# Kernel optimization log

Hardware: AMD Instinct MI355X
Metric: run time of the kernel (lower is better)

The kernel has to match this reference:

```python
import jax, jax.numpy as jnp
import numpy as np

P = 7            # POOL_SIZE
NUM_CLASSES = 20
STRIDE = 16      # FEATURE_STRIDE
SCALE = 1.0 / STRIDE
C_IN = 512
C_MID = 2 * C_IN
C_CLS = P * P * (NUM_CLASSES + 1)        # 1029
C_BOX = P * P * (NUM_CLASSES + 1) * 4    # 4116
H, W = 38, 50
K = 300
IMG_H, IMG_W = 600.0, 800.0


def conv1x1(w, b, x):
    # w: [Cout, Cin], b: [Cout], x: [Cin, H, W] -> ReLU(conv) (CNNBlock = Conv2d 1x1 + ReLU)
    return jax.nn.relu(jnp.einsum('oi,ihw->ohw', w, x) + b[:, None, None])


def ps_roi_pool(maps, rois_xyxy):
    # maps: [Ctot, H, W] with Ctot = Cout*P*P, channel index = (c*P + ph)*P + pw
    # rois_xyxy: [K, 4] (x1, y1, x2, y2) in image coords. torchvision PSRoIPool math.
    Ctot, h, w = maps.shape
    Cout = Ctot // (P * P)
    x1 = jnp.round(rois_xyxy[:, 0]) * SCALE
    y1 = jnp.round(rois_xyxy[:, 1]) * SCALE
    x2 = (jnp.round(rois_xyxy[:, 2]) + 1.0) * SCALE
    y2 = (jnp.round(rois_xyxy[:, 3]) + 1.0) * SCALE
    roi_w = jnp.maximum(x2 - x1, 0.1)
    roi_h = jnp.maximum(y2 - y1, 0.1)
    bin_w = roi_w / P
    bin_h = roi_h / P
    i = jnp.arange(P, dtype=maps.dtype)
    hs = jnp.clip(jnp.floor(y1[:, None] + bin_h[:, None] * i), 0.0, h)        # [K,P]
    he = jnp.clip(jnp.ceil(y1[:, None] + bin_h[:, None] * (i + 1.0)), 0.0, h)
    ws = jnp.clip(jnp.floor(x1[:, None] + bin_w[:, None] * i), 0.0, w)
    we = jnp.clip(jnp.ceil(x1[:, None] + bin_w[:, None] * (i + 1.0)), 0.0, w)
    hidx = jnp.arange(h, dtype=maps.dtype)
    widx = jnp.arange(w, dtype=maps.dtype)
    hmask = ((hidx >= hs[..., None]) & (hidx < he[..., None])).astype(maps.dtype)  # [K,P,H]
    wmask = ((widx >= ws[..., None]) & (widx < we[..., None])).astype(maps.dtype)  # [K,P,W]
    maps_r = maps.reshape(Cout, P, P, h, w)
    t = jnp.einsum('cijhw,kih->kcijw', maps_r, hmask)     # reduce over h
    s = jnp.einsum('kcijw,kjw->kcij', t, wmask)           # reduce over w -> [K,Cout,P,P]
    cnt = ((he - hs)[:, :, None] * (we - ws)[:, None, :])[:, None]  # [K,1,P,P]
    return jnp.where(cnt > 0, s / jnp.maximum(cnt, 1.0), 0.0)


def setup_inputs() -> dict:
    key = jax.random.key(0)
    ks = jax.random.split(key, 10)
    feature = jax.random.normal(ks[0], (C_IN, H, W), dtype=jnp.float32)
    # rois in (y1, x1, y2, x2) image coords, matching the column permute in forward
    ymin = jax.random.uniform(ks[1], (K,), minval=0.0, maxval=IMG_H - 32.0)
    xmin = jax.random.uniform(ks[2], (K,), minval=0.0, maxval=IMG_W - 32.0)
    yh = jax.random.uniform(ks[3], (K,), minval=16.0, maxval=256.0)
    xw = jax.random.uniform(ks[4], (K,), minval=16.0, maxval=256.0)
    ymax = jnp.minimum(ymin + yh, IMG_H - 1.0)
    xmax = jnp.minimum(xmin + xw, IMG_W - 1.0)
    rois = jnp.stack([ymin, xmin, ymax, xmax], axis=1)
    sd1 = 1.0 / np.sqrt(C_IN)
    sd2 = 1.0 / np.sqrt(C_MID)
    w_double = jax.random.normal(ks[5], (C_MID, C_IN), dtype=jnp.float32) * sd1
    b_double = jnp.zeros((C_MID,), dtype=jnp.float32)
    w_score = jax.random.normal(ks[6], (C_CLS, C_MID), dtype=jnp.float32) * sd2
    b_score = jnp.zeros((C_CLS,), dtype=jnp.float32)
    w_bbox = jax.random.normal(ks[7], (C_BOX, C_MID), dtype=jnp.float32) * sd2
    b_bbox = jnp.zeros((C_BOX,), dtype=jnp.float32)
    return {"feature": feature, "rois": rois,
            "w_double": w_double, "b_double": b_double,
            "w_score": w_score, "b_score": b_score,
            "w_bbox": w_bbox, "b_bbox": b_bbox}


def reference(feature, rois, w_double, b_double, w_score, b_score, w_bbox, b_bbox):
    feat2 = conv1x1(w_double, b_double, feature)               # [2C, H, W]
    # rois given as (y1,x1,y2,x2) -> (x1,y1,x2,y2), per xy_indices_and_rois permute
    rois_xyxy = rois[:, jnp.array([1, 0, 3, 2])]
    score_maps = conv1x1(w_score, b_score, feat2)              # [P*P*(NC+1), H, W]
    class_vote = ps_roi_pool(score_maps, rois_xyxy)            # [K, NC+1, P, P]
    predicted_roi_score = jnp.mean(class_vote, axis=(-2, -1))  # AvgPool2d(P) + squeeze -> [K, NC+1]
    bbox_maps = conv1x1(w_bbox, b_bbox, feat2)                 # [P*P*(NC+1)*4, H, W]
    bbox_vote = ps_roi_pool(bbox_maps, rois_xyxy)              # [K, 4*(NC+1), P, P]
    predicted_roi_offset = jnp.mean(bbox_vote, axis=(-2, -1))  # [K, 4*(NC+1)]
    return predicted_roi_score, predicted_roi_offset
```

## Files before the change

kernel.cpp:

```cpp
#include <hip/hip_runtime.h>
#include <hip/hip_bf16.h>

#define P 7
#define C_IN 512
#define C_MID 1024
#define C_CLS 1029
#define C_BOX 4116
#define FH 38
#define FW 50
#define NPIX 1900
#define KROIS 300
#define COUT_SCORE 21
#define COUT_BOX 84
#define NPAIRS (KROIS * (COUT_SCORE + COUT_BOX))

#define MP1 1024
#define MP2 1152
#define MP3 4224
#define NPAD 1920

__device__ unsigned short g_w1h[MP1 * C_IN],  g_w1l[MP1 * C_IN];
__device__ unsigned short g_w2h[MP2 * C_MID], g_w2l[MP2 * C_MID];
__device__ unsigned short g_w3h[MP3 * C_MID], g_w3l[MP3 * C_MID];
__device__ unsigned short g_fTh[NPAD * C_IN], g_fTl[NPAD * C_IN];
__device__ unsigned short g_f2Th[NPAD * C_MID], g_f2Tl[NPAD * C_MID];
__device__ float g_score[C_CLS * NPIX];
__device__ float g_bbox [C_BOX * NPIX];

typedef __attribute__((ext_vector_type(8))) short bf16x8;
typedef __attribute__((ext_vector_type(4))) float f32x4;

__device__ __forceinline__ unsigned short f2b(float x) {
    unsigned u = __float_as_uint(x);
    unsigned r = u + 0x7fffu + ((u >> 16) & 1u);
    return (unsigned short)(r >> 16);
}
__device__ __forceinline__ float b2f(unsigned short h) {
    return __uint_as_float((unsigned)h << 16);
}

#define GLOAD16(gp, lp)                                                        \
    __builtin_amdgcn_global_load_lds(                                          \
        (const __attribute__((address_space(1))) void*)(gp),                   \
        (__attribute__((address_space(3))) void*)(lp), 16, 0, 0)

__global__ __launch_bounds__(256) void split_pad_k(
    const float* __restrict__ src,
    unsigned short* __restrict__ h, unsigned short* __restrict__ l,
    int n_in4, int n_pad4)
{
    const int i = blockIdx.x * 256 + threadIdx.x;
    if (i >= n_pad4) return;
    float4 v = make_float4(0.f, 0.f, 0.f, 0.f);
    if (i < n_in4) v = reinterpret_cast<const float4*>(src)[i];
    ushort4 hh, lv;
    hh.x = f2b(v.x); lv.x = f2b(v.x - b2f(hh.x));
    hh.y = f2b(v.y); lv.y = f2b(v.y - b2f(hh.y));
    hh.z = f2b(v.z); lv.z = f2b(v.z - b2f(hh.z));
    hh.w = f2b(v.w); lv.w = f2b(v.w - b2f(hh.w));
    reinterpret_cast<ushort4*>(h)[i] = hh;
    reinterpret_cast<ushort4*>(l)[i] = lv;
}

__global__ __launch_bounds__(256) void transpose_split_k(const float* __restrict__ in)
{
    __shared__ float t[32][33];
    const int n0 = blockIdx.x * 32;
    const int k0 = blockIdx.y * 32;
    const int tx = threadIdx.x & 31;
    const int ty = threadIdx.x >> 5;
    #pragma unroll
    for (int j = 0; j < 4; ++j) {
        const int kk = k0 + ty + j * 8;
        const int nn = n0 + tx;
        t[ty + j * 8][tx] = (nn < NPIX) ? in[kk * NPIX + nn] : 0.f;
    }
    __syncthreads();
    #pragma unroll
    for (int j = 0; j < 4; ++j) {
        const int nn = n0 + ty + j * 8;
        const int kk = k0 + tx;
        const float v = t[tx][ty + j * 8];
        const unsigned short hh = f2b(v);
        g_fTh[(size_t)nn * C_IN + kk] = hh;
        g_fTl[(size_t)nn * C_IN + kk] = f2b(v - b2f(hh));
    }
}

template <bool TROUT>
__global__ __launch_bounds__(256) void gemm_mfma(
    const unsigned short* __restrict__ Ah, const unsigned short* __restrict__ Al,
    const unsigned short* __restrict__ Bh, const unsigned short* __restrict__ Bl,
    const float* __restrict__ bias,
    float* __restrict__ out,
    unsigned short* __restrict__ outh,
    unsigned short* __restrict__ outl,
    int M, int K, int N)
{
    __shared__ unsigned char lds[65536];

    const int tid = threadIdx.x;
    const int bm = blockIdx.y * 128;
    const int bn = blockIdx.x * 128;
    const int lane = tid & 63;
    const int wid = tid >> 6;
    const int uwid = __builtin_amdgcn_readfirstlane(wid);
    const int wr = (wid >> 1) * 64;
    const int wc = (wid & 1) * 64;
    const int ll = lane & 15;
    const int lg = lane >> 4;
    const int lh4 = lg * 4;

    const int lrow = lane >> 3;
    const int lseg = (lane & 7) ^ lrow;
    const unsigned short* gsrc = (uwid == 0) ? Ah : (uwid == 1) ? Al : (uwid == 2) ? Bh : Bl;
    const int rbase = (uwid < 2) ? bm : bn;
    unsigned char* lplane = &lds[uwid * 16384];

    f32x4 acc[4][4];
    #pragma unroll
    for (int i = 0; i < 4; ++i)
        #pragma unroll
        for (int j = 0; j < 4; ++j) {
            f32x4 z = {0.f, 0.f, 0.f, 0.f};
            acc[i][j] = z;
        }

    const unsigned char* pAh = &lds[0];
    const unsigned char* pAl = &lds[16384];
    const unsigned char* pBh = &lds[32768];
    const unsigned char* pBl = &lds[49152];

    for (int k0 = 0; k0 < K; k0 += 64) {
        const unsigned short* gp = gsrc + (size_t)(rbase + lrow) * K + lseg * 8 + k0;
        #pragma unroll
        for (int g = 0; g < 16; ++g)
            GLOAD16(gp + (size_t)g * 8 * K, lplane + g * 1024);
        asm volatile("s_waitcnt vmcnt(0)" ::: "memory");
        __syncthreads();

        #pragma unroll
        for (int kh = 0; kh < 2; ++kh) {
            const int slot = kh * 4 + lg;
            bf16x8 bh[4], bl[4];
            #pragma unroll
            for (int nt = 0; nt < 4; ++nt) {
                const int r = wc + nt * 16 + ll;
                const int so = ((slot ^ (r & 7)) << 4);
                bh[nt] = *reinterpret_cast<const bf16x8*>(pBh + r * 128 + so);
                bl[nt] = *reinterpret_cast<const bf16x8*>(pBl + r * 128 + so);
            }
            #pragma unroll
            for (int mt = 0; mt < 4; ++mt) {
                const int r = wr + mt * 16 + ll;
                const int so = ((slot ^ (r & 7)) << 4);
                const bf16x8 ah = *reinterpret_cast<const bf16x8*>(pAh + r * 128 + so);
                const bf16x8 al = *reinterpret_cast<const bf16x8*>(pAl + r * 128 + so);
                #pragma unroll
                for (int nt = 0; nt < 4; ++nt) {
                    acc[mt][nt] = __builtin_amdgcn_mfma_f32_16x16x32_bf16(ah, bh[nt], acc[mt][nt], 0, 0, 0);
                    acc[mt][nt] = __builtin_amdgcn_mfma_f32_16x16x32_bf16(ah, bl[nt], acc[mt][nt], 0, 0, 0);
                    acc[mt][nt] = __builtin_amdgcn_mfma_f32_16x16x32_bf16(al, bh[nt], acc[mt][nt], 0, 0, 0);
                }
            }
        }
        __syncthreads();
    }

    #pragma unroll
    for (int mt = 0; mt < 4; ++mt) {
        #pragma unroll
        for (int nt = 0; nt < 4; ++nt) {
            const int m0 = bm + wr + mt * 16 + lh4;
            const int n  = bn + wc + nt * 16 + ll;
            if (TROUT) {
                float o0 = fmaxf(acc[mt][nt][0] + bias[m0 + 0], 0.f);
                float o1 = fmaxf(acc[mt][nt][1] + bias[m0 + 1], 0.f);
                float o2 = fmaxf(acc[mt][nt][2] + bias[m0 + 2], 0.f);
                float o3 = fmaxf(acc[mt][nt][3] + bias[m0 + 3], 0.f);
                ushort4 hh, lv;
                hh.x = f2b(o0); lv.x = f2b(o0 - b2f(hh.x));
                hh.y = f2b(o1); lv.y = f2b(o1 - b2f(hh.y));
                hh.z = f2b(o2); lv.z = f2b(o2 - b2f(hh.z));
                hh.w = f2b(o3); lv.w = f2b(o3 - b2f(hh.w));
                *reinterpret_cast<ushort4*>(&outh[(size_t)n * M + m0]) = hh;
                *reinterpret_cast<ushort4*>(&outl[(size_t)n * M + m0]) = lv;
            } else {
                #pragma unroll
                for (int r = 0; r < 4; ++r) {
                    const int m = m0 + r;
                    if (m < M && n < N)
                        out[(size_t)m * N + n] = fmaxf(acc[mt][nt][r] + bias[m], 0.f);
                }
            }
        }
    }
}

__global__ __launch_bounds__(256) void psroi_pool_mean(
    const float* __restrict__ rois, float* __restrict__ out)
{
    __shared__ float red[4][64];
    const int wid = threadIdx.x >> 6;
    const int lane = threadIdx.x & 63;
    const int pair = blockIdx.x * 4 + wid;

    const int k = pair / (COUT_SCORE + COUT_BOX);
    const int c = pair % (COUT_SCORE + COUT_BOX);

    const float* maps;
    int cbase;
    float* outp;
    if (c < COUT_SCORE) {
        maps = g_score;
        cbase = c * (P * P);
        outp = out + (size_t)k * COUT_SCORE + c;
    } else {
        const int cb = c - COUT_SCORE;
        maps = g_bbox;
        cbase = cb * (P * P);
        outp = out + (size_t)KROIS * COUT_SCORE + (size_t)k * COUT_BOX + cb;
    }

    const float ymin = rois[k * 4 + 0];
    const float xmin = rois[k * 4 + 1];
    const float ymax = rois[k * 4 + 2];
    const float xmax = rois[k * 4 + 3];

    const float x1 = __fmul_rn(rintf(xmin), 0.0625f);
    const float y1 = __fmul_rn(rintf(ymin), 0.0625f);
    const float x2 = __fmul_rn(__fadd_rn(rintf(xmax), 1.0f), 0.0625f);
    const float y2 = __fmul_rn(__fadd_rn(rintf(ymax), 1.0f), 0.0625f);
    const float roi_w = fmaxf(__fsub_rn(x2, x1), 0.1f);
    const float roi_h = fmaxf(__fsub_rn(y2, y1), 0.1f);
    const float inv7 = 1.0f / 7.0f;
    const float bin_w = __fmul_rn(roi_w, inv7);
    const float bin_h = __fmul_rn(roi_h, inv7);

    float val = 0.f;
    if (lane < P * P) {
        const int i = lane / P;
        const int j = lane % P;
        const float hs = fminf(fmaxf(floorf(__fadd_rn(y1, __fmul_rn(bin_h, (float)i))), 0.f), (float)FH);
        const float he = fminf(fmaxf(ceilf (__fadd_rn(y1, __fmul_rn(bin_h, (float)(i + 1)))), 0.f), (float)FH);
        const float wsb = fminf(fmaxf(floorf(__fadd_rn(x1, __fmul_rn(bin_w, (float)j))), 0.f), (float)FW);
        const float web = fminf(fmaxf(ceilf (__fadd_rn(x1, __fmul_rn(bin_w, (float)(j + 1)))), 0.f), (float)FW);
        const float cnt = __fmul_rn(__fsub_rn(he, hs), __fsub_rn(web, wsb));
        if (cnt > 0.f) {
            const int ys = (int)hs, ye = (int)he, xs = (int)wsb, xe = (int)web;
            const int rows = ye - ys, cols = xe - xs;
            const float* mp = maps + (size_t)(cbase + lane) * NPIX;
            float s = 0.f;
            if (rows <= 4 && cols <= 4) {
                #pragma unroll
                for (int t = 0; t < 16; ++t) {
                    const int dy = t >> 2, dx = t & 3;
                    const float v = (dy < rows && dx < cols)
                                        ? mp[(ys + dy) * FW + (xs + dx)] : 0.f;
                    s += v;
                }
            } else {
                for (int y = ys; y < ye; ++y)
                    for (int x = xs; x < xe; ++x)
                        s += mp[y * FW + x];
            }
            val = s / fmaxf(cnt, 1.0f);
        }
    }

    red[wid][lane] = val;
    __syncthreads();

    if (lane == 0) {
        float s = 0.f;
        for (int l = 0; l < P * P; ++l) s += red[wid][l];
        *outp = s * (1.0f / 49.0f);
    }
}

extern "C" void kernel_launch(void* const* d_in, const int* in_sizes, int n_in,
                              void* d_out, int out_size, void* d_ws, size_t ws_size,
                              hipStream_t stream) {
    const float* feature  = (const float*)d_in[0];
    const float* rois     = (const float*)d_in[1];
    const float* w_double = (const float*)d_in[2];
    const float* b_double = (const float*)d_in[3];
    const float* w_score  = (const float*)d_in[4];
    const float* b_score  = (const float*)d_in[5];
    const float* w_bbox   = (const float*)d_in[6];
    const float* b_bbox   = (const float*)d_in[7];
    float* out = (float*)d_out;

    unsigned short *w1h, *w1l, *w2h, *w2l, *w3h, *w3l, *fTh, *fTl, *f2Th, *f2Tl;
    float *scoreM, *bboxM;
    hipGetSymbolAddress((void**)&w1h,  HIP_SYMBOL(g_w1h));
    hipGetSymbolAddress((void**)&w1l,  HIP_SYMBOL(g_w1l));
    hipGetSymbolAddress((void**)&w2h,  HIP_SYMBOL(g_w2h));
    hipGetSymbolAddress((void**)&w2l,  HIP_SYMBOL(g_w2l));
    hipGetSymbolAddress((void**)&w3h,  HIP_SYMBOL(g_w3h));
    hipGetSymbolAddress((void**)&w3l,  HIP_SYMBOL(g_w3l));
    hipGetSymbolAddress((void**)&fTh,  HIP_SYMBOL(g_fTh));
    hipGetSymbolAddress((void**)&fTl,  HIP_SYMBOL(g_fTl));
    hipGetSymbolAddress((void**)&f2Th, HIP_SYMBOL(g_f2Th));
    hipGetSymbolAddress((void**)&f2Tl, HIP_SYMBOL(g_f2Tl));
    hipGetSymbolAddress((void**)&scoreM, HIP_SYMBOL(g_score));
    hipGetSymbolAddress((void**)&bboxM,  HIP_SYMBOL(g_bbox));

    const dim3 blk(256);

    split_pad_k<<<(MP1 * C_IN / 4 + 255) / 256, blk, 0, stream>>>(
        w_double, w1h, w1l, C_MID * C_IN / 4, MP1 * C_IN / 4);
    split_pad_k<<<(MP2 * C_MID / 4 + 255) / 256, blk, 0, stream>>>(
        w_score, w2h, w2l, C_CLS * C_MID / 4, MP2 * C_MID / 4);
    split_pad_k<<<(MP3 * C_MID / 4 + 255) / 256, blk, 0, stream>>>(
        w_bbox, w3h, w3l, C_BOX * C_MID / 4, MP3 * C_MID / 4);

    transpose_split_k<<<dim3(NPAD / 32, C_IN / 32), blk, 0, stream>>>(feature);

    gemm_mfma<true ><<<dim3(NPAD / 128, MP1 / 128), blk, 0, stream>>>(
        w1h, w1l, fTh, fTl, b_double, nullptr, f2Th, f2Tl, C_MID, C_IN, NPIX);

    gemm_mfma<false><<<dim3(NPAD / 128, MP2 / 128), blk, 0, stream>>>(
        w2h, w2l, f2Th, f2Tl, b_score, scoreM, nullptr, nullptr, C_CLS, C_MID, NPIX);
    gemm_mfma<false><<<dim3(NPAD / 128, MP3 / 128), blk, 0, stream>>>(
        w3h, w3l, f2Th, f2Tl, b_bbox, bboxM, nullptr, nullptr, C_BOX, C_MID, NPIX);

    psroi_pool_mean<<<dim3(NPAIRS / 4), blk, 0, stream>>>(rois, out);
}
```

Measured before the change: 218.4 us.

## Merge score/bbox GEMMs with permuted weights, double-buffer K loop, coalesce PSRoI reads

The score and bbox weight matrices are permuted into one bin-major matrix (bin, class-channel) with a combined bias, so a single GEMM writes pixel-major maps where the 105 channels of each bin are contiguous. The PSRoI pool then has one thread per channel, looping over bins, and reads coalesced across channels instead of strided per-channel maps. The GEMM K loop now uses a 32-wide step with double-buffered LDS staging to overlap global loads with MFMA work. Risks include smaller K tiles meaning more barriers, and a pool kernel with only 150 blocks and a serial 49-bin loop.

```diff
diff --git a/kernel.cpp b/kernel.cpp
--- a/kernel.cpp
+++ b/kernel.cpp
@@ -12,20 +12,19 @@
 #define KROIS 300
 #define COUT_SCORE 21
 #define COUT_BOX 84
-#define NPAIRS (KROIS * (COUT_SCORE + COUT_BOX))
+#define COUT_ALL 105
 
 #define MP1 1024
-#define MP2 1152
-#define MP3 4224
+#define MPC 5248
+#define MC_REAL 5145
 #define NPAD 1920
 
 __device__ unsigned short g_w1h[MP1 * C_IN],  g_w1l[MP1 * C_IN];
-__device__ unsigned short g_w2h[MP2 * C_MID], g_w2l[MP2 * C_MID];
-__device__ unsigned short g_w3h[MP3 * C_MID], g_w3l[MP3 * C_MID];
-__device__ unsigned short g_fTh[NPAD * C_IN], g_fTl[NPAD * C_IN];
+__device__ unsigned short g_wch[MPC * C_MID], g_wcl[MPC * C_MID];
+__device__ float          g_biasc[MPC];
+__device__ unsigned short g_fTh[NPAD * C_IN],  g_fTl[NPAD * C_IN];
 __device__ unsigned short g_f2Th[NPAD * C_MID], g_f2Tl[NPAD * C_MID];
-__device__ float g_score[C_CLS * NPIX];
-__device__ float g_bbox [C_BOX * NPIX];
+__device__ float g_mapsT[(size_t)NPAD * MPC];
 
 typedef __attribute__((ext_vector_type(8))) short bf16x8;
 typedef __attribute__((ext_vector_type(4))) float f32x4;
@@ -62,6 +61,43 @@
     reinterpret_cast<ushort4*>(l)[i] = lv;
 }
 
+__global__ __launch_bounds__(256) void permute_split_k(
+    const float* __restrict__ ws, const float* __restrict__ wb,
+    const float* __restrict__ bs, const float* __restrict__ bb,
+    unsigned short* __restrict__ h, unsigned short* __restrict__ l,
+    float* __restrict__ biasp)
+{
+    const int idx = blockIdx.x * 256 + threadIdx.x;
+    const int m = idx >> 7;
+    const int ko = (idx & 127) * 8;
+    if (m >= MPC) return;
+    float v[8] = {0.f, 0.f, 0.f, 0.f, 0.f, 0.f, 0.f, 0.f};
+    float bv = 0.f;
+    if (m < MC_REAL) {
+        const int b = m / COUT_ALL, c = m % COUT_ALL;
+        const float* src;
+        if (c < COUT_SCORE) { const int r = c * 49 + b;                src = ws + (size_t)r * C_MID; bv = bs[r]; }
+        else                { const int r = (c - COUT_SCORE) * 49 + b; src = wb + (size_t)r * C_MID; bv = bb[r]; }
+        const float4 a0 = *reinterpret_cast<const float4*>(src + ko);
+        const float4 a1 = *reinterpret_cast<const float4*>(src + ko + 4);
+        v[0] = a0.x; v[1] = a0.y; v[2] = a0.z; v[3] = a0.w;
+        v[4] = a1.x; v[5] = a1.y; v[6] = a1.z; v[7] = a1.w;
+    }
+    ushort4 hh0, hh1, lv0, lv1;
+    unsigned short th[8], tl[8];
+    #pragma unroll
+    for (int q = 0; q < 8; ++q) { th[q] = f2b(v[q]); tl[q] = f2b(v[q] - b2f(th[q])); }
+    hh0 = make_ushort4(th[0], th[1], th[2], th[3]);
+    hh1 = make_ushort4(th[4], th[5], th[6], th[7]);
+    lv0 = make_ushort4(tl[0], tl[1], tl[2], tl[3]);
+    lv1 = make_ushort4(tl[4], tl[5], tl[6], tl[7]);
+    reinterpret_cast<ushort4*>(h + (size_t)m * C_MID + ko)[0] = hh0;
+    reinterpret_cast<ushort4*>(h + (size_t)m * C_MID + ko)[1] = hh1;
+    reinterpret_cast<ushort4*>(l + (size_t)m * C_MID + ko)[0] = lv0;
+    reinterpret_cast<ushort4*>(l + (size_t)m * C_MID + ko)[1] = lv1;
+    if (ko == 0) biasp[m] = bv;
+}
+
 __global__ __launch_bounds__(256) void transpose_split_k(const float* __restrict__ in)
 {
     __shared__ float t[32][33];
@@ -87,15 +123,14 @@
     }
 }
 
-template <bool TROUT>
+template <int OUT_MODE>
 __global__ __launch_bounds__(256) void gemm_mfma(
     const unsigned short* __restrict__ Ah, const unsigned short* __restrict__ Al,
     const unsigned short* __restrict__ Bh, const unsigned short* __restrict__ Bl,
     const float* __restrict__ bias,
-    float* __restrict__ out,
-    unsigned short* __restrict__ outh,
-    unsigned short* __restrict__ outl,
-    int M, int K, int N)
+    float* __restrict__ outf,
+    unsigned short* __restrict__ outh, unsigned short* __restrict__ outl,
+    int M, int K)
 {
     __shared__ unsigned char lds[65536];
 
@@ -111,11 +146,11 @@
     const int lg = lane >> 4;
     const int lh4 = lg * 4;
 
-    const int lrow = lane >> 3;
-    const int lseg = (lane & 7) ^ lrow;
+    const int lrow = lane >> 2;
+    const int lseg = (lane & 3) ^ (lrow & 3);
     const unsigned short* gsrc = (uwid == 0) ? Ah : (uwid == 1) ? Al : (uwid == 2) ? Bh : Bl;
     const int rbase = (uwid < 2) ? bm : bn;
-    unsigned char* lplane = &lds[uwid * 16384];
+    const size_t grow = (size_t)(rbase + lrow) * K + lseg * 8;
 
     f32x4 acc[4][4];
     #pragma unroll
@@ -126,45 +161,52 @@
             acc[i][j] = z;
         }
 
-    const unsigned char* pAh = &lds[0];
-    const unsigned char* pAl = &lds[16384];
-    const unsigned char* pBh = &lds[32768];
-    const unsigned char* pBl = &lds[49152];
-
-    for (int k0 = 0; k0 < K; k0 += 64) {
-        const unsigned short* gp = gsrc + (size_t)(rbase + lrow) * K + lseg * 8 + k0;
-        #pragma unroll
-        for (int g = 0; g < 16; ++g)
-            GLOAD16(gp + (size_t)g * 8 * K, lplane + g * 1024);
+    auto STAGE = [&](int buf, int k0) {
+        const unsigned short* gp = gsrc + grow + k0;
+        unsigned char* lp = &lds[buf * 32768 + uwid * 8192];
+        #pragma unroll
+        for (int g = 0; g < 8; ++g)
+            GLOAD16(gp + (size_t)g * 16 * K, lp + g * 1024);
+    };
+
+    STAGE(0, 0);
+    asm volatile("s_waitcnt vmcnt(0)" ::: "memory");
+    __syncthreads();
+
+    int cur = 0;
+    for (int k0 = 0; k0 < K; k0 += 32) {
+        if (k0 + 32 < K) STAGE(cur ^ 1, k0 + 32);
+
+        const unsigned char* base = &lds[cur * 32768];
+        const unsigned char* pAh = base;
+        const unsigned char* pAl = base + 8192;
+        const unsigned char* pBh = base + 16384;
+        const unsigned char* pBl = base + 24576;
+
+        bf16x8 bh[4], bl[4];
+        #pragma unroll
+        for (int nt = 0; nt < 4; ++nt) {
+            const int r = wc + nt * 16 + ll;
+            const int off = r * 64 + ((lg ^ (r & 3)) << 4);
+            bh[nt] = *reinterpret_cast<const bf16x8*>(pBh + off);
+            bl[nt] = *reinterpret_cast<const bf16x8*>(pBl + off);
+        }
+        #pragma unroll
+        for (int mt = 0; mt < 4; ++mt) {
+            const int r = wr + mt * 16 + ll;
+            const int off = r * 64 + ((lg ^ (r & 3)) << 4);
+            const bf16x8 ah = *reinterpret_cast<const bf16x8*>(pAh + off);
+            const bf16x8 al = *reinterpret_cast<const bf16x8*>(pAl + off);
+            #pragma unroll
+            for (int nt = 0; nt < 4; ++nt) {
+                acc[mt][nt] = __builtin_amdgcn_mfma_f32_16x16x32_bf16(ah, bh[nt], acc[mt][nt], 0, 0, 0);
+                acc[mt][nt] = __builtin_amdgcn_mfma_f32_16x16x32_bf16(ah, bl[nt], acc[mt][nt], 0, 0, 0);
+                acc[mt][nt] = __builtin_amdgcn_mfma_f32_16x16x32_bf16(al, bh[nt], acc[mt][nt], 0, 0, 0);
+            }
+        }
         asm volatile("s_waitcnt vmcnt(0)" ::: "memory");
         __syncthreads();
-
-        #pragma unroll
-        for (int kh = 0; kh < 2; ++kh) {
-            const int slot = kh * 4 + lg;
-            bf16x8 bh[4], bl[4];
-            #pragma unroll
-            for (int nt = 0; nt < 4; ++nt) {
-                const int r = wc + nt * 16 + ll;
-                const int so = ((slot ^ (r & 7)) << 4);
-                bh[nt] = *reinterpret_cast<const bf16x8*>(pBh + r * 128 + so);
-                bl[nt] = *reinterpret_cast<const bf16x8*>(pBl + r * 128 + so);
-            }
-            #pragma unroll
-            for (int mt = 0; mt < 4; ++mt) {
-                const int r = wr + mt * 16 + ll;
-                const int so = ((slot ^ (r & 7)) << 4);
-                const bf16x8 ah = *reinterpret_cast<const bf16x8*>(pAh + r * 128 + so);
-                const bf16x8 al = *reinterpret_cast<const bf16x8*>(pAl + r * 128 + so);
-                #pragma unroll
-                for (int nt = 0; nt < 4; ++nt) {
-                    acc[mt][nt] = __builtin_amdgcn_mfma_f32_16x16x32_bf16(ah, bh[nt], acc[mt][nt], 0, 0, 0);
-                    acc[mt][nt] = __builtin_amdgcn_mfma_f32_16x16x32_bf16(ah, bl[nt], acc[mt][nt], 0, 0, 0);
-                    acc[mt][nt] = __builtin_amdgcn_mfma_f32_16x16x32_bf16(al, bh[nt], acc[mt][nt], 0, 0, 0);
-                }
-            }
-        }
-        __syncthreads();
+        cur ^= 1;
     }
 
     #pragma unroll
@@ -173,11 +215,14 @@
         for (int nt = 0; nt < 4; ++nt) {
             const int m0 = bm + wr + mt * 16 + lh4;
             const int n  = bn + wc + nt * 16 + ll;
-            if (TROUT) {
-                float o0 = fmaxf(acc[mt][nt][0] + bias[m0 + 0], 0.f);
-                float o1 = fmaxf(acc[mt][nt][1] + bias[m0 + 1], 0.f);
-                float o2 = fmaxf(acc[mt][nt][2] + bias[m0 + 2], 0.f);
-                float o3 = fmaxf(acc[mt][nt][3] + bias[m0 + 3], 0.f);
+            const float o0 = fmaxf(acc[mt][nt][0] + bias[m0 + 0], 0.f);
+            const float o1 = fmaxf(acc[mt][nt][1] + bias[m0 + 1], 0.f);
+            const float o2 = fmaxf(acc[mt][nt][2] + bias[m0 + 2], 0.f);
+            const float o3 = fmaxf(acc[mt][nt][3] + bias[m0 + 3], 0.f);
+            if (OUT_MODE == 0) {
+                float4 o = make_float4(o0, o1, o2, o3);
+                *reinterpret_cast<float4*>(&outf[(size_t)n * M + m0]) = o;
+            } else {
                 ushort4 hh, lv;
                 hh.x = f2b(o0); lv.x = f2b(o0 - b2f(hh.x));
                 hh.y = f2b(o1); lv.y = f2b(o1 - b2f(hh.y));
@@ -185,42 +230,18 @@
                 hh.w = f2b(o3); lv.w = f2b(o3 - b2f(hh.w));
                 *reinterpret_cast<ushort4*>(&outh[(size_t)n * M + m0]) = hh;
                 *reinterpret_cast<ushort4*>(&outl[(size_t)n * M + m0]) = lv;
-            } else {
-                #pragma unroll
-                for (int r = 0; r < 4; ++r) {
-                    const int m = m0 + r;
-                    if (m < M && n < N)
-                        out[(size_t)m * N + n] = fmaxf(acc[mt][nt][r] + bias[m], 0.f);
-                }
             }
         }
     }
 }
 
 __global__ __launch_bounds__(256) void psroi_pool_mean(
-    const float* __restrict__ rois, float* __restrict__ out)
-{
-    __shared__ float red[4][64];
-    const int wid = threadIdx.x >> 6;
-    const int lane = threadIdx.x & 63;
-    const int pair = blockIdx.x * 4 + wid;
-
-    const int k = pair / (COUT_SCORE + COUT_BOX);
-    const int c = pair % (COUT_SCORE + COUT_BOX);
-
-    const float* maps;
-    int cbase;
-    float* outp;
-    if (c < COUT_SCORE) {
-        maps = g_score;
-        cbase = c * (P * P);
-        outp = out + (size_t)k * COUT_SCORE + c;
-    } else {
-        const int cb = c - COUT_SCORE;
-        maps = g_bbox;
-        cbase = cb * (P * P);
-        outp = out + (size_t)KROIS * COUT_SCORE + (size_t)k * COUT_BOX + cb;
-    }
+    const float* __restrict__ rois, const float* __restrict__ mapsT,
+    float* __restrict__ out)
+{
+    const int half = threadIdx.x >> 7;
+    const int c = threadIdx.x & 127;
+    const int k = blockIdx.x * 2 + half;
 
     const float ymin = rois[k * 4 + 0];
     const float xmin = rois[k * 4 + 1];
@@ -237,44 +258,32 @@
     const float bin_w = __fmul_rn(roi_w, inv7);
     const float bin_h = __fmul_rn(roi_h, inv7);
 
-    float val = 0.f;
-    if (lane < P * P) {
-        const int i = lane / P;
-        const int j = lane % P;
+    float tot = 0.f;
+    for (int b = 0; b < 49; ++b) {
+        const int i = b / 7;
+        const int j = b % 7;
         const float hs = fminf(fmaxf(floorf(__fadd_rn(y1, __fmul_rn(bin_h, (float)i))), 0.f), (float)FH);
         const float he = fminf(fmaxf(ceilf (__fadd_rn(y1, __fmul_rn(bin_h, (float)(i + 1)))), 0.f), (float)FH);
         const float wsb = fminf(fmaxf(floorf(__fadd_rn(x1, __fmul_rn(bin_w, (float)j))), 0.f), (float)FW);
         const float web = fminf(fmaxf(ceilf (__fadd_rn(x1, __fmul_rn(bin_w, (float)(j + 1)))), 0.f), (float)FW);
         const float cnt = __fmul_rn(__fsub_rn(he, hs), __fsub_rn(web, wsb));
+        float val = 0.f;
         if (cnt > 0.f) {
             const int ys = (int)hs, ye = (int)he, xs = (int)wsb, xe = (int)web;
-            const int rows = ye - ys, cols = xe - xs;
-            const float* mp = maps + (size_t)(cbase + lane) * NPIX;
+            const float* mb = mapsT + (size_t)b * COUT_ALL + c;
             float s = 0.f;
-            if (rows <= 4 && cols <= 4) {
-                #pragma unroll
-                for (int t = 0; t < 16; ++t) {
-                    const int dy = t >> 2, dx = t & 3;
-                    const float v = (dy < rows && dx < cols)
-                                        ? mp[(ys + dy) * FW + (xs + dx)] : 0.f;
-                    s += v;
-                }
-            } else {
-                for (int y = ys; y < ye; ++y)
-                    for (int x = xs; x < xe; ++x)
-                        s += mp[y * FW + x];
-            }
+            for (int y = ys; y < ye; ++y)
+                for (int x = xs; x < xe; ++x)
+                    s += mb[(size_t)(y * FW + x) * MPC];
             val = s / fmaxf(cnt, 1.0f);
         }
-    }
-
-    red[wid][lane] = val;
-    __syncthreads();
-
-    if (lane == 0) {
-        float s = 0.f;
-        for (int l = 0; l < P * P; ++l) s += red[wid][l];
-        *outp = s * (1.0f / 49.0f);
+        tot += val;
+    }
+
+    if (c < COUT_ALL) {
+        const float r = tot * (1.0f / 49.0f);
+        if (c < COUT_SCORE) out[(size_t)k * COUT_SCORE + c] = r;
+        else out[(size_t)KROIS * COUT_SCORE + (size_t)k * COUT_BOX + (c - COUT_SCORE)] = r;
     }
 }
 
@@ -291,39 +300,34 @@
     const float* b_bbox   = (const float*)d_in[7];
     float* out = (float*)d_out;
 
-    unsigned short *w1h, *w1l, *w2h, *w2l, *w3h, *w3l, *fTh, *fTl, *f2Th, *f2Tl;
-    float *scoreM, *bboxM;
-    hipGetSymbolAddress((void**)&w1h,  HIP_SYMBOL(g_w1h));
-    hipGetSymbolAddress((void**)&w1l,  HIP_SYMBOL(g_w1l));
-    hipGetSymbolAddress((void**)&w2h,  HIP_SYMBOL(g_w2h));
-    hipGetSymbolAddress((void**)&w2l,  HIP_SYMBOL(g_w2l));
-    hipGetSymbolAddress((void**)&w3h,  HIP_SYMBOL(g_w3h));
-    hipGetSymbolAddress((void**)&w3l,  HIP_SYMBOL(g_w3l));
-    hipGetSymbolAddress((void**)&fTh,  HIP_SYMBOL(g_fTh));
-    hipGetSymbolAddress((void**)&fTl,  HIP_SYMBOL(g_fTl));
-    hipGetSymbolAddress((void**)&f2Th, HIP_SYMBOL(g_f2Th));
-    hipGetSymbolAddress((void**)&f2Tl, HIP_SYMBOL(g_f2Tl));
-    hipGetSymbolAddress((void**)&scoreM, HIP_SYMBOL(g_score));
-    hipGetSymbolAddress((void**)&bboxM,  HIP_SYMBOL(g_bbox));
+    unsigned short *w1h, *w1l, *wch, *wcl, *fTh, *fTl, *f2Th, *f2Tl;
+    float *biasc, *mapsT;
+    hipGetSymbolAddress((void**)&w1h,   HIP_SYMBOL(g_w1h));
+    hipGetSymbolAddress((void**)&w1l,   HIP_SYMBOL(g_w1l));
+    hipGetSymbolAddress((void**)&wch,   HIP_SYMBOL(g_wch));
+    hipGetSymbolAddress((void**)&wcl,   HIP_SYMBOL(g_wcl));
+    hipGetSymbolAddress((void**)&biasc, HIP_SYMBOL(g_biasc));
+    hipGetSymbolAddress((void**)&fTh,   HIP_SYMBOL(g_fTh));
+    hipGetSymbolAddress((void**)&fTl,   HIP_SYMBOL(g_fTl));
+    hipGetSymbolAddress((void**)&f2Th,  HIP_SYMBOL(g_f2Th));
+    hipGetSymbolAddress((void**)&f2Tl,  HIP_SYMBOL(g_f2Tl));
+    hipGetSymbolAddress((void**)&mapsT, HIP_SYMBOL(g_mapsT));
 
     const dim3 blk(256);
 
     split_pad_k<<<(MP1 * C_IN / 4 + 255) / 256, blk, 0, stream>>>(
         w_double, w1h, w1l, C_MID * C_IN / 4, MP1 * C_IN / 4);
-    split_pad_k<<<(MP2 * C_MID / 4 + 255) / 256, blk, 0, stream>>>(
-        w_score, w2h, w2l, C_CLS * C_MID / 4, MP2 * C_MID / 4);
-    split_pad_k<<<(MP3 * C_MID / 4 + 255) / 256, blk, 0, stream>>>(
-        w_bbox, w3h, w3l, C_BOX * C_MID / 4, MP3 * C_MID / 4);
+
+    permute_split_k<<<(MPC * (C_MID / 8) + 255) / 256, blk, 0, stream>>>(
+        w_score, w_bbox, b_score, b_bbox, wch, wcl, biasc);
 
     transpose_split_k<<<dim3(NPAD / 32, C_IN / 32), blk, 0, stream>>>(feature);
 
-    gemm_mfma<true ><<<dim3(NPAD / 128, MP1 / 128), blk, 0, stream>>>(
-        w1h, w1l, fTh, fTl, b_double, nullptr, f2Th, f2Tl, C_MID, C_IN, NPIX);
-
-    gemm_mfma<false><<<dim3(NPAD / 128, MP2 / 128), blk, 0, stream>>>(
-        w2h, w2l, f2Th, f2Tl, b_score, scoreM, nullptr, nullptr, C_CLS, C_MID, NPIX);
-    gemm_mfma<false><<<dim3(NPAD / 128, MP3 / 128), blk, 0, stream>>>(
-        w3h, w3l, f2Th, f2Tl, b_bbox, bboxM, nullptr, nullptr, C_BOX, C_MID, NPIX);
-
-    psroi_pool_mean<<<dim3(NPAIRS / 4), blk, 0, stream>>>(rois, out);
-}
+    gemm_mfma<1><<<dim3(NPAD / 128, MP1 / 128), blk, 0, stream>>>(
+        w1h, w1l, fTh, fTl, b_double, nullptr, f2Th, f2Tl, MP1, C_IN);
+
+    gemm_mfma<0><<<dim3(NPAD / 128, MPC / 128), blk, 0, stream>>>(
+        wch, wcl, f2Th, f2Tl, biasc, mapsT, nullptr, nullptr, MPC, C_MID);
+
+    psroi_pool_mean<<<dim3(KROIS / 2), blk, 0, stream>>>(rois, mapsT, out);
+}
```

Result: slower. 284.1 us (+30.1%).
